# Kernel optimization log

Measured on AMD Instinct MI355X. Metric: run time of the kernel, lower is better.

Reference implementation:

```python
import jax, jax.numpy as jnp
import numpy as np

N_NODES = 100000
N_EDGES = 1600000
IN_CH = 128
HID = 32
HEADS = 4
OUT_CH = 32
NEG_SLOPE = 0.2  # PyG GATConv default


def setup_inputs() -> dict:
    key = jax.random.key(0)
    ks = jax.random.split(key, 12)
    s = 0.1
    x = jax.random.normal(ks[0], (N_NODES, IN_CH), dtype=jnp.float32)
    edge_index = jax.random.randint(ks[1], (2, N_EDGES), 0, N_NODES, dtype=jnp.int64)
    # layer 1: in -> heads*hid, concat
    W1 = jax.random.normal(ks[2], (IN_CH, HEADS * HID), dtype=jnp.float32) * s
    a_src1 = jax.random.normal(ks[3], (HEADS, HID), dtype=jnp.float32) * s
    a_dst1 = jax.random.normal(ks[4], (HEADS, HID), dtype=jnp.float32) * s
    b1 = jnp.zeros((HEADS * HID,), dtype=jnp.float32)
    # layer 2: heads*hid -> out, single head, averaged
    W2 = jax.random.normal(ks[5], (HEADS * HID, OUT_CH), dtype=jnp.float32) * s
    a_src2 = jax.random.normal(ks[6], (1, OUT_CH), dtype=jnp.float32) * s
    a_dst2 = jax.random.normal(ks[7], (1, OUT_CH), dtype=jnp.float32) * s
    b2 = jnp.zeros((OUT_CH,), dtype=jnp.float32)
    return {"x": x, "edge_index": edge_index, "W1": W1, "a_src1": a_src1,
            "a_dst1": a_dst1, "b1": b1, "W2": W2, "a_src2": a_src2,
            "a_dst2": a_dst2, "b2": b2}


def _gat_layer(x, src, dst, W, a_s, a_d, b, heads, ch, concat):
    n = x.shape[0]
    h = (x @ W).reshape(n, heads, ch)            # [N,H,C]
    alpha_s = jnp.einsum('nhc,hc->nh', h, a_s)   # [N,H]
    alpha_d = jnp.einsum('nhc,hc->nh', h, a_d)
    e = jax.nn.leaky_relu(alpha_s[src] + alpha_d[dst], NEG_SLOPE)  # [E,H]
    # segment softmax over edges sharing a destination (self-loops guarantee
    # every segment is non-empty)
    m = jax.ops.segment_max(e, dst, num_segments=n)
    ex = jnp.exp(e - m[dst])
    denom = jax.ops.segment_sum(ex, dst, num_segments=n)
    alpha = ex / (denom[dst] + 1e-16)            # [E,H]
    out = jax.ops.segment_sum(alpha[:, :, None] * h[src], dst, num_segments=n)  # [N,H,C]
    out = out.reshape(n, heads * ch) if concat else out.mean(axis=1)
    return out + b


def reference(x, edge_index, W1, a_src1, a_dst1, b1, W2, a_src2, a_dst2, b2):
    n = x.shape[0]
    loop = jnp.arange(n, dtype=edge_index.dtype)
    src = jnp.concatenate([edge_index[0], loop])  # add self-loops (PyG default)
    dst = jnp.concatenate([edge_index[1], loop])
    h = _gat_layer(x, src, dst, W1, a_src1, a_dst1, b1, HEADS, HID, True)
    h = jax.nn.relu(h)
    # dropout(p=0.5) is identity in eval mode
    out = _gat_layer(h, src, dst, W2, a_src2, a_dst2, b2, 1, OUT_CH, False)
    return out
```

## Files before the change

kernel.cpp:

```cpp
#include <hip/hip_runtime.h>
#include <math.h>

#define NEG_SLOPE 0.2f
#define EPB 8192

typedef __attribute__((ext_vector_type(8))) short bf16x8;
typedef __attribute__((ext_vector_type(4))) float f32x4;

__device__ __forceinline__ unsigned pack_bf16x2(float a, float b) {
    unsigned ua = __float_as_uint(a);
    unsigned ub = __float_as_uint(b);
    ua += 0x7FFFu + ((ua >> 16) & 1u);
    ub += 0x7FFFu + ((ub >> 16) & 1u);
    return (ua >> 16) | (ub & 0xFFFF0000u);
}
__device__ __forceinline__ unsigned short bf16r(float f) {
    unsigned u = __float_as_uint(f);
    u += 0x7FFFu + ((u >> 16) & 1u);
    return (unsigned short)(u >> 16);
}
__device__ __forceinline__ float bf_lo(unsigned u) { return __uint_as_float(u << 16); }
__device__ __forceinline__ float bf_hi(unsigned u) { return __uint_as_float(u & 0xFFFF0000u); }

#if defined(__has_builtin)
#if __has_builtin(__builtin_amdgcn_make_buffer_rsrc) && \
    __has_builtin(__builtin_amdgcn_raw_ptr_buffer_load_b32) && \
    __has_builtin(__builtin_amdgcn_raw_ptr_buffer_load_b64)
#define USE_BUFLD 1
#endif
#endif

#ifdef USE_BUFLD
typedef __amdgpu_buffer_rsrc_t Rsrc;
typedef __attribute__((ext_vector_type(2))) unsigned uint2v;
__device__ __forceinline__ Rsrc mkrsrc(const void* p) {
    return __builtin_amdgcn_make_buffer_rsrc((void*)p, (short)0, -1, 0x00020000);
}
__device__ __forceinline__ unsigned bufld_u32(Rsrc r, int voff) {
    return __builtin_amdgcn_raw_ptr_buffer_load_b32(r, voff, 0, 0);
}
__device__ __forceinline__ float bufld_f32(Rsrc r, int voff) {
    return __uint_as_float(__builtin_amdgcn_raw_ptr_buffer_load_b32(r, voff, 0, 0));
}
__device__ __forceinline__ uint2 bufld_u64(Rsrc r, int voff) {
    uint2v v = __builtin_amdgcn_raw_ptr_buffer_load_b64(r, voff, 0, 0);
    return make_uint2(v.x, v.y);
}
#else
struct Rsrc { const char* p; };
__device__ __forceinline__ Rsrc mkrsrc(const void* p) { Rsrc r; r.p = (const char*)p; return r; }
__device__ __forceinline__ unsigned bufld_u32(Rsrc r, int voff) { return *(const unsigned*)(r.p + voff); }
__device__ __forceinline__ float bufld_f32(Rsrc r, int voff) { return *(const float*)(r.p + voff); }
__device__ __forceinline__ uint2 bufld_u64(Rsrc r, int voff) { return *(const uint2*)(r.p + voff); }
#endif

#define SWZ(row, byteoff) ((((row) * 256) + (byteoff)) ^ (((row) & 15) << 4))


__global__ __launch_bounds__(256) void wcvt_kernel(const float* __restrict__ W,
                                                   unsigned short* __restrict__ WT,
                                                   int Nc, int total) {
    int id = blockIdx.x * 256 + threadIdx.x;
    if (id < total) {
        int n = id >> 7, k = id & 127;
        WT[id] = bf16r(W[k * Nc + n]);
    }
}


__global__ __launch_bounds__(256) void gscan_bsum(const int* __restrict__ arr,
                                                  int* __restrict__ psum, int M) {
    __shared__ int red[4];
    int tid = threadIdx.x;
    int idx = blockIdx.x * 256 + tid;
    int v = (idx < M) ? arr[idx] : 0;
    #pragma unroll
    for (int off = 1; off < 64; off <<= 1) v += __shfl_xor(v, off, 64);
    if ((tid & 63) == 0) red[tid >> 6] = v;
    __syncthreads();
    if (tid == 0) psum[blockIdx.x] = red[0] + red[1] + red[2] + red[3];
}

__global__ __launch_bounds__(1024) void gscan_psum(int* __restrict__ psum, int nb) {
    __shared__ int ws[16];
    int tid = threadIdx.x, lane = tid & 63, w = tid >> 6;
    int v = (tid < nb) ? psum[tid] : 0;
    int incl = v;
    #pragma unroll
    for (int off = 1; off < 64; off <<= 1) {
        int t = __shfl_up(incl, off, 64);
        if (lane >= off) incl += t;
    }
    if (lane == 63) ws[w] = incl;
    __syncthreads();
    int wbase = 0;
    #pragma unroll
    for (int j = 0; j < 16; j++) { if (j < w) wbase += ws[j]; }
    if (tid < nb) psum[tid] = wbase + incl - v;
}

__global__ __launch_bounds__(256) void gscan_final(int* __restrict__ arr,
                                                   const int* __restrict__ psum, int M) {
    __shared__ int ws[4];
    int tid = threadIdx.x, lane = tid & 63, w = tid >> 6;
    int idx = blockIdx.x * 256 + tid;
    int v = (idx < M) ? arr[idx] : 0;
    int incl = v;
    #pragma unroll
    for (int off = 1; off < 64; off <<= 1) {
        int t = __shfl_up(incl, off, 64);
        if (lane >= off) incl += t;
    }
    if (lane == 63) ws[w] = incl;
    __syncthreads();
    int wbase = 0;
    #pragma unroll
    for (int j = 0; j < 4; j++) { if (j < w) wbase += ws[j]; }
    if (idx < M) arr[idx] = psum[blockIdx.x] + wbase + incl - v;
}


__global__ __launch_bounds__(256) void p1_hist(const int* __restrict__ dst, int E, int N,
                                               int nblk1, int nbuckets,
                                               int* __restrict__ partial) {
    __shared__ int hist[1024];
    int tid = threadIdx.x;
    for (int i = tid; i < nbuckets; i += 256) hist[i] = 0;
    __syncthreads();
    int base = blockIdx.x * EPB;
    int tot = E + N;
    #pragma unroll
    for (int it = 0; it < EPB / 256; it++) {
        int i = base + it * 256 + tid;
        if (i < tot) {
            int d = (i < E) ? dst[i] : (i - E);
            atomicAdd(&hist[d >> 8], 1);
        }
    }
    __syncthreads();
    for (int b = tid; b < nbuckets; b += 256)
        partial[b * nblk1 + blockIdx.x] = hist[b];
}

__global__ __launch_bounds__(256) void p1_scatter(const int* __restrict__ src,
                                                  const int* __restrict__ dst, int E, int N,
                                                  int nblk1, int nbuckets,
                                                  const int* __restrict__ scanned,
                                                  unsigned* __restrict__ pairs) {
    __shared__ int cursor[1024];
    int tid = threadIdx.x;
    for (int b = tid; b < nbuckets; b += 256)
        cursor[b] = scanned[b * nblk1 + blockIdx.x];
    __syncthreads();
    int base = blockIdx.x * EPB;
    int tot = E + N;
    #pragma unroll
    for (int it = 0; it < EPB / 256; it++) {
        int i = base + it * 256 + tid;
        if (i < tot) {
            int s = (i < E) ? src[i] : (i - E);
            int d = (i < E) ? dst[i] : (i - E);
            int pos = atomicAdd(&cursor[d >> 8], 1);
            pairs[pos] = ((unsigned)(d & 255) << 24) | (unsigned)s;
        }
    }
}

#define P2CAP 8192

__global__ __launch_bounds__(256) void p2_kernel(const unsigned* __restrict__ pairs,
                                                 const int* __restrict__ scanned,
                                                 int nblk1, int nbuckets, int Etot, int N,
                                                 int* __restrict__ rowptr,
                                                 int* __restrict__ col) {
    __shared__ unsigned buf[P2CAP];
    __shared__ int cnt[256];
    __shared__ int cur[256];
    __shared__ int wsum[4];
    int b = blockIdx.x;
    int tid = threadIdx.x, lane = tid & 63, w = tid >> 6;
    int bucketStart = scanned[b * nblk1];
    int bucketEnd = (b + 1 < nbuckets) ? scanned[(b + 1) * nblk1] : Etot;
    int sz = bucketEnd - bucketStart;
    bool inLds = (sz <= P2CAP);
    cnt[tid] = 0;
    if (inLds) {
        for (int i = tid; i < sz; i += 256) buf[i] = pairs[bucketStart + i];
    }
    __syncthreads();
    if (inLds) {
        for (int i = tid; i < sz; i += 256) atomicAdd(&cnt[buf[i] >> 24], 1);
    } else {
        for (int i = bucketStart + tid; i < bucketEnd; i += 256)
            atomicAdd(&cnt[pairs[i] >> 24], 1);
    }
    __syncthreads();
    int v = cnt[tid];
    int incl = v;
    #pragma unroll
    for (int off = 1; off < 64; off <<= 1) {
        int t = __shfl_up(incl, off, 64);
        if (lane >= off) incl += t;
    }
    if (lane == 63) wsum[w] = incl;
    __syncthreads();
    int wbase = 0;
    #pragma unroll
    for (int j = 0; j < 4; j++) { if (j < w) wbase += wsum[j]; }
    int base = bucketStart + wbase + incl - v;
    cur[tid] = base;
    int d = b * 256 + tid;
    if (d < N) rowptr[d] = base;
    if (b == nbuckets - 1 && tid == 0) rowptr[N] = Etot;
    __syncthreads();
    if (inLds) {
        for (int i = tid; i < sz; i += 256) {
            unsigned p = buf[i];
            int pos = atomicAdd(&cur[p >> 24], 1);
            col[pos] = (int)(p & 0xFFFFFFu);
        }
    } else {
        for (int i = bucketStart + tid; i < bucketEnd; i += 256) {
            unsigned p = pairs[i];
            int pos = atomicAdd(&cur[p >> 24], 1);
            col[pos] = (int)(p & 0xFFFFFFu);
        }
    }
}


__global__ __launch_bounds__(256) void exk_kernel(const int* __restrict__ rowptr,
                                                  const int* __restrict__ col,
                                                  const float* __restrict__ as1,
                                                  const float4* __restrict__ ad4,
                                                  float* __restrict__ exh,
                                                  int N, int Etot) {
    int lane = threadIdx.x & 63;
    int wid = __builtin_amdgcn_readfirstlane(threadIdx.x >> 6);
    int n = blockIdx.x * 4 + wid;
    if (n >= N) return;
    int h = lane >> 4, jj = lane & 15;
    float4 D = ad4[n];
    float dn = (h < 2) ? (h == 0 ? D.x : D.y) : (h == 2 ? D.z : D.w);
    int beg = rowptr[n], end = rowptr[n + 1];
    int planeBase = h * Etot;
    for (int i = beg; i < end; i += 16) {
        int e = i + jj;
        if (e < end) {
            int s = col[e];
            float a = as1[s * 4 + h];
            float v = a + dn;
            v = fmaxf(v, v * NEG_SLOPE);
            exh[planeBase + e] = __expf(v);
        }
    }
}


__global__ __launch_bounds__(256) void gemm1_kernel(const float* __restrict__ x,
                                                    const unsigned short* __restrict__ W1T,
                                                    const float* __restrict__ a_s,
                                                    const float* __restrict__ a_d,
                                                    uint4* __restrict__ h1b,
                                                    float* __restrict__ as1,
                                                    float* __restrict__ ad1, int N) {
    __shared__ char xs[16384];
    __shared__ char wsm[32768];
    int tid = threadIdx.x;
    int row0 = blockIdx.x * 64;

    #pragma unroll
    for (int it = 0; it < 8; it++) {
        int idx = it * 256 + tid;
        int n = idx >> 4, kq = idx & 15;
        uint4 v = ((const uint4*)W1T)[idx];
        *(uint4*)(wsm + SWZ(n, kq * 16)) = v;
    }
    #pragma unroll
    for (int it = 0; it < 8; it++) {
        int idx = it * 256 + tid;
        int r = idx >> 5, k4 = idx & 31;
        int row = row0 + r;
        float4 v = (row < N) ? ((const float4*)x)[(size_t)row * 32 + k4]
                             : make_float4(0.f, 0.f, 0.f, 0.f);
        uint2 p;
        p.x = pack_bf16x2(v.x, v.y);
        p.y = pack_bf16x2(v.z, v.w);
        *(uint2*)(xs + SWZ(r, k4 * 8)) = p;
    }
    __syncthreads();

    int wv = tid >> 6, lane = tid & 63;
    int r0 = wv * 16;
    int lm = lane & 15, lk = lane >> 4;

    bf16x8 afr[4];
    #pragma unroll
    for (int ks = 0; ks < 4; ks++) {
        int row = r0 + lm;
        afr[ks] = *(const bf16x8*)(xs + SWZ(row, ks * 64 + lk * 16));
    }
    f32x4 acc[8];
    #pragma unroll
    for (int nt = 0; nt < 8; nt++) acc[nt] = (f32x4){0.f, 0.f, 0.f, 0.f};

    #pragma unroll
    for (int nt = 0; nt < 8; nt++) {
        int c = nt * 16 + lm;
        #pragma unroll
        for (int ks = 0; ks < 4; ks++) {
            bf16x8 bfr = *(const bf16x8*)(wsm + SWZ(c, ks * 64 + lk * 16));
            acc[nt] = __builtin_amdgcn_mfma_f32_16x16x32_bf16(afr[ks], bfr, acc[nt], 0, 0, 0);
        }
    }
    __syncthreads();

    #pragma unroll
    for (int nt = 0; nt < 8; nt++) {
        int c = nt * 16 + lm;
        #pragma unroll
        for (int e = 0; e < 4; e++) {
            int row = r0 + lk * 4 + e;
            *(unsigned short*)(xs + SWZ(row, c * 2)) = bf16r(acc[nt][e]);
        }
    }
    __syncthreads();

    #pragma unroll
    for (int it = 0; it < 4; it++) {
        int idx = it * 256 + tid;
        int row = idx >> 4, q = idx & 15;
        if (row0 + row < N) {
            uint4 v = *(const uint4*)(xs + SWZ(row, q * 16));
            h1b[(size_t)(row0 + row) * 16 + q] = v;
        }
    }
    {
        int row = tid >> 2, h = tid & 3;
        if (row0 + row < N) {
            float sd = 0.f, dd = 0.f;
            #pragma unroll
            for (int q = 0; q < 4; q++) {
                uint4 v = *(const uint4*)(xs + SWZ(row, h * 64 + q * 16));
                unsigned uu[4] = {v.x, v.y, v.z, v.w};
                #pragma unroll
                for (int j = 0; j < 4; j++) {
                    int k = h * 32 + q * 8 + 2 * j;
                    sd = fmaf(bf_lo(uu[j]), a_s[k], sd);
                    sd = fmaf(bf_hi(uu[j]), a_s[k + 1], sd);
                    dd = fmaf(bf_lo(uu[j]), a_d[k], dd);
                    dd = fmaf(bf_hi(uu[j]), a_d[k + 1], dd);
                }
            }
            as1[(row0 + row) * 4 + h] = sd;
            ad1[(row0 + row) * 4 + h] = dd;
        }
    }
}


__global__ __launch_bounds__(256) void agg1_kernel(const int* __restrict__ rowptr,
                                                   const int* __restrict__ col,
                                                   const unsigned* __restrict__ h1b,
                                                   const float* __restrict__ exh,
                                                   const float* __restrict__ b1,
                                                   unsigned* __restrict__ out1b,
                                                   int N, int Etot) {
    int lane = threadIdx.x & 63;
    int wid = __builtin_amdgcn_readfirstlane(threadIdx.x >> 6);
    int n = blockIdx.x * 4 + wid;
    if (n >= N) return;
    int hh = lane >> 4;
    Rsrc h1r = mkrsrc(h1b);
    Rsrc exr = mkrsrc(exh);
    int laneByte = lane << 2;
    int exBase = hh * Etot;
    int beg = rowptr[n], end = rowptr[n + 1];
    float ax0 = 0.f, ay0 = 0.f, d0 = 0.f;
    float ax1 = 0.f, ay1 = 0.f, d1 = 0.f;
    float ax2 = 0.f, ay2 = 0.f, d2 = 0.f;
    float ax3 = 0.f, ay3 = 0.f, d3 = 0.f;
    int i = beg;
    for (; i + 16 <= end; i += 16) {
        unsigned uu[16];
        float ex[16];
        #pragma unroll
        for (int j = 0; j < 16; j++) {
            int s = col[i + j];
            uu[j] = bufld_u32(h1r, (s << 8) + laneByte);
            ex[j] = bufld_f32(exr, (exBase + i + j) << 2);
        }
        #pragma unroll
        for (int j = 0; j < 16; j += 4) {
            d0 += ex[j];     ax0 = fmaf(ex[j],     bf_lo(uu[j]),     ax0); ay0 = fmaf(ex[j],     bf_hi(uu[j]),     ay0);
            d1 += ex[j + 1]; ax1 = fmaf(ex[j + 1], bf_lo(uu[j + 1]), ax1); ay1 = fmaf(ex[j + 1], bf_hi(uu[j + 1]), ay1);
            d2 += ex[j + 2]; ax2 = fmaf(ex[j + 2], bf_lo(uu[j + 2]), ax2); ay2 = fmaf(ex[j + 2], bf_hi(uu[j + 2]), ay2);
            d3 += ex[j + 3]; ax3 = fmaf(ex[j + 3], bf_lo(uu[j + 3]), ax3); ay3 = fmaf(ex[j + 3], bf_hi(uu[j + 3]), ay3);
        }
    }
    for (; i + 4 <= end; i += 4) {
        unsigned uu[4];
        float ex[4];
        #pragma unroll
        for (int j = 0; j < 4; j++) {
            int s = col[i + j];
            uu[j] = bufld_u32(h1r, (s << 8) + laneByte);
            ex[j] = bufld_f32(exr, (exBase + i + j) << 2);
        }
        d0 += ex[0]; ax0 = fmaf(ex[0], bf_lo(uu[0]), ax0); ay0 = fmaf(ex[0], bf_hi(uu[0]), ay0);
        d1 += ex[1]; ax1 = fmaf(ex[1], bf_lo(uu[1]), ax1); ay1 = fmaf(ex[1], bf_hi(uu[1]), ay1);
        d2 += ex[2]; ax2 = fmaf(ex[2], bf_lo(uu[2]), ax2); ay2 = fmaf(ex[2], bf_hi(uu[2]), ay2);
        d3 += ex[3]; ax3 = fmaf(ex[3], bf_lo(uu[3]), ax3); ay3 = fmaf(ex[3], bf_hi(uu[3]), ay3);
    }
    for (; i < end; i++) {
        int s = col[i];
        unsigned u = bufld_u32(h1r, (s << 8) + laneByte);
        float x = bufld_f32(exr, (exBase + i) << 2);
        d0 += x;
        ax0 = fmaf(x, bf_lo(u), ax0);
        ay0 = fmaf(x, bf_hi(u), ay0);
    }
    float den = (d0 + d1) + (d2 + d3);
    float ax = (ax0 + ax1) + (ax2 + ax3);
    float ay = (ay0 + ay1) + (ay2 + ay3);
    float2 bb = ((const float2*)b1)[lane];
    float ox = fmaxf(ax / den + bb.x, 0.f);
    float oy = fmaxf(ay / den + bb.y, 0.f);
    out1b[n * 64 + lane] = pack_bf16x2(ox, oy);
}


__global__ __launch_bounds__(256) void gemm2_kernel(const uint4* __restrict__ out1b,
                                                    const unsigned short* __restrict__ W2T,
                                                    const float* __restrict__ a_s,
                                                    const float* __restrict__ a_d,
                                                    uint4* __restrict__ h2b,
                                                    float* __restrict__ as2,
                                                    float* __restrict__ ad2, int N) {
    __shared__ char xs[16384];
    __shared__ char wsm[8192];
    int tid = threadIdx.x;
    int row0 = blockIdx.x * 64;

    #pragma unroll
    for (int it = 0; it < 2; it++) {
        int idx = it * 256 + tid;
        int n = idx >> 4, kq = idx & 15;
        uint4 v = ((const uint4*)W2T)[idx];
        *(uint4*)(wsm + SWZ(n, kq * 16)) = v;
    }
    #pragma unroll
    for (int it = 0; it < 4; it++) {
        int idx = it * 256 + tid;
        int r = idx >> 4, q = idx & 15;
        int row = row0 + r;
        uint4 v = (row < N) ? out1b[(size_t)row * 16 + q] : make_uint4(0, 0, 0, 0);
        *(uint4*)(xs + SWZ(r, q * 16)) = v;
    }
    __syncthreads();

    int wv = tid >> 6, lane = tid & 63;
    int r0 = wv * 16;
    int lm = lane & 15, lk = lane >> 4;

    bf16x8 afr[4];
    #pragma unroll
    for (int ks = 0; ks < 4; ks++) {
        int row = r0 + lm;
        afr[ks] = *(const bf16x8*)(xs + SWZ(row, ks * 64 + lk * 16));
    }
    f32x4 acc[2];
    acc[0] = (f32x4){0.f, 0.f, 0.f, 0.f};
    acc[1] = (f32x4){0.f, 0.f, 0.f, 0.f};
    #pragma unroll
    for (int nt = 0; nt < 2; nt++) {
        int c = nt * 16 + lm;
        #pragma unroll
        for (int ks = 0; ks < 4; ks++) {
            bf16x8 bfr = *(const bf16x8*)(wsm + SWZ(c, ks * 64 + lk * 16));
            acc[nt] = __builtin_amdgcn_mfma_f32_16x16x32_bf16(afr[ks], bfr, acc[nt], 0, 0, 0);
        }
    }
    __syncthreads();

    #pragma unroll
    for (int nt = 0; nt < 2; nt++) {
        int c = nt * 16 + lm;
        #pragma unroll
        for (int e = 0; e < 4; e++) {
            int row = r0 + lk * 4 + e;
            *(unsigned short*)(xs + SWZ(row, c * 2)) = bf16r(acc[nt][e]);
        }
    }
    __syncthreads();

    {
        int row = tid >> 2, q = tid & 3;
        if (row0 + row < N) {
            uint4 v = *(const uint4*)(xs + SWZ(row, q * 16));
            h2b[(size_t)(row0 + row) * 4 + q] = v;
        }
    }
    if (tid < 64 && row0 + tid < N) {
        float sd = 0.f, dd = 0.f;
        #pragma unroll
        for (int q = 0; q < 4; q++) {
            uint4 v = *(const uint4*)(xs + SWZ(tid, q * 16));
            unsigned uu[4] = {v.x, v.y, v.z, v.w};
            #pragma unroll
            for (int j = 0; j < 4; j++) {
                int k = q * 8 + 2 * j;
                sd = fmaf(bf_lo(uu[j]), a_s[k], sd);
                sd = fmaf(bf_hi(uu[j]), a_s[k + 1], sd);
                dd = fmaf(bf_lo(uu[j]), a_d[k], dd);
                dd = fmaf(bf_hi(uu[j]), a_d[k + 1], dd);
            }
        }
        as2[row0 + tid] = sd;
        ad2[row0 + tid] = dd;
    }
}


#define A2SLOT(u, l)                                               \
    {                                                              \
        float e = l + adn;                                         \
        e = fmaxf(e, e * NEG_SLOPE);                               \
        float ex = __expf(e);                                      \
        den += ex;                                                 \
        a0 = fmaf(ex, bf_lo(u.x), a0);                             \
        a1 = fmaf(ex, bf_hi(u.x), a1);                             \
        a2 = fmaf(ex, bf_lo(u.y), a2);                             \
        a3 = fmaf(ex, bf_hi(u.y), a3);                             \
    }

__global__ __launch_bounds__(256) void agg2_kernel(const int* __restrict__ rowptr,
                                                   const int* __restrict__ col,
                                                   const unsigned* __restrict__ h2b,
                                                   const float* __restrict__ as2,
                                                   const float* __restrict__ ad2,
                                                   const float* __restrict__ b2,
                                                   float* __restrict__ out, int N) {
    int lane = threadIdx.x & 63;
    int wid = __builtin_amdgcn_readfirstlane(threadIdx.x >> 6);
    int n = blockIdx.x * 4 + wid;
    if (n >= N) return;
    int q8 = lane >> 3;
    int cl = lane & 7;
    Rsrc h2r = mkrsrc(h2b);
    Rsrc asr = mkrsrc(as2);
    int clByte = cl << 3;
    float adn = ad2[n];
    int beg = rowptr[n], end = rowptr[n + 1];
    float a0 = 0.f, a1 = 0.f, a2 = 0.f, a3 = 0.f, den = 0.f;
    int i = beg;
    for (; i + 16 <= end; i += 16) {
        int e0 = i + q8, e1 = i + 8 + q8;
        int s0 = col[e0], s1 = col[e1];
        uint2 u0 = bufld_u64(h2r, (s0 << 6) + clByte);
        uint2 u1 = bufld_u64(h2r, (s1 << 6) + clByte);
        float l0 = bufld_f32(asr, s0 << 2);
        float l1 = bufld_f32(asr, s1 << 2);
        A2SLOT(u0, l0) A2SLOT(u1, l1)
    }
    for (; i < end; i += 8) {
        int e = i + q8;
        if (e < end) {
            int s = col[e];
            uint2 u = bufld_u64(h2r, (s << 6) + clByte);
            float l = bufld_f32(asr, s << 2);
            A2SLOT(u, l)
        }
    }
    den += __shfl_xor(den, 8, 64);
    den += __shfl_xor(den, 16, 64);
    den += __shfl_xor(den, 32, 64);
    a0 += __shfl_xor(a0, 8, 64);  a0 += __shfl_xor(a0, 16, 64);  a0 += __shfl_xor(a0, 32, 64);
    a1 += __shfl_xor(a1, 8, 64);  a1 += __shfl_xor(a1, 16, 64);  a1 += __shfl_xor(a1, 32, 64);
    a2 += __shfl_xor(a2, 8, 64);  a2 += __shfl_xor(a2, 16, 64);  a2 += __shfl_xor(a2, 32, 64);
    a3 += __shfl_xor(a3, 8, 64);  a3 += __shfl_xor(a3, 16, 64);  a3 += __shfl_xor(a3, 32, 64);
    if (q8 == 0) {
        float4 bb = ((const float4*)b2)[cl];
        float4 o;
        o.x = a0 / den + bb.x;
        o.y = a1 / den + bb.y;
        o.z = a2 / den + bb.z;
        o.w = a3 / den + bb.w;
        ((float4*)out)[n * 8 + cl] = o;
    }
}


extern "C" void kernel_launch(void* const* d_in, const int* in_sizes, int n_in,
                              void* d_out, int out_size, void* d_ws, size_t ws_size,
                              hipStream_t stream) {
    const float* x    = (const float*)d_in[0];
    const int*   ei   = (const int*)d_in[1];
    const float* W1   = (const float*)d_in[2];
    const float* a_s1 = (const float*)d_in[3];
    const float* a_d1 = (const float*)d_in[4];
    const float* b1   = (const float*)d_in[5];
    const float* W2   = (const float*)d_in[6];
    const float* a_s2 = (const float*)d_in[7];
    const float* a_d2 = (const float*)d_in[8];
    const float* b2   = (const float*)d_in[9];

    int N = in_sizes[0] / 128;
    int E = in_sizes[1] / 2;
    const int* srcA = ei;
    const int* dstA = ei + E;
    int Etot = E + N;

    char* ws = (char*)d_ws;
    size_t off = 0;
    auto alloc = [&](size_t bytes) {
        void* p = ws + off;
        off += (bytes + 255) & ~(size_t)255;
        return p;
    };
    unsigned* h1b   = (unsigned*)alloc((size_t)N * 128 * 2);
    unsigned* out1b = (unsigned*)alloc((size_t)N * 128 * 2);
    unsigned* h2b   = (unsigned*)alloc((size_t)N * 32 * 2);
    float* as1      = (float*)alloc((size_t)N * 4 * 4);
    float* ad1      = (float*)alloc((size_t)N * 4 * 4);
    float* as2      = (float*)alloc((size_t)N * 4);
    float* ad2      = (float*)alloc((size_t)N * 4);
    int*   rowptr   = (int*)alloc((size_t)(N + 1) * 4);
    int*   col      = (int*)alloc((size_t)Etot * 4);
    unsigned* pairs = (unsigned*)alloc((size_t)Etot * 4);
    float* exh      = (float*)alloc((size_t)Etot * 4 * 4);
    unsigned short* W1T = (unsigned short*)alloc(128 * 128 * 2);
    unsigned short* W2T = (unsigned short*)alloc(32 * 128 * 2);

    int nbuckets = (N + 255) >> 8;
    int nblk1 = (Etot + EPB - 1) / EPB;
    int M = nbuckets * nblk1;
    int*   partial = (int*)alloc((size_t)M * 4);
    int nbs = (M + 255) / 256;
    int*   psum    = (int*)alloc((size_t)1024 * 4);

    hipLaunchKernelGGL(wcvt_kernel, dim3(64), dim3(256), 0, stream, W1, W1T, 128, 16384);
    hipLaunchKernelGGL(wcvt_kernel, dim3(16), dim3(256), 0, stream, W2, W2T, 32, 4096);
    hipLaunchKernelGGL(gemm1_kernel, dim3((N + 63) / 64), dim3(256), 0, stream,
                       x, W1T, a_s1, a_d1, (uint4*)h1b, as1, ad1, N);

    hipLaunchKernelGGL(p1_hist, dim3(nblk1), dim3(256), 0, stream,
                       dstA, E, N, nblk1, nbuckets, partial);
    hipLaunchKernelGGL(gscan_bsum, dim3(nbs), dim3(256), 0, stream, partial, psum, M);
    hipLaunchKernelGGL(gscan_psum, dim3(1), dim3(1024), 0, stream, psum, nbs);
    hipLaunchKernelGGL(gscan_final, dim3(nbs), dim3(256), 0, stream, partial, psum, M);
    hipLaunchKernelGGL(p1_scatter, dim3(nblk1), dim3(256), 0, stream,
                       srcA, dstA, E, N, nblk1, nbuckets, partial, pairs);
    hipLaunchKernelGGL(p2_kernel, dim3(nbuckets), dim3(256), 0, stream,
                       pairs, partial, nblk1, nbuckets, Etot, N, rowptr, col);

    hipLaunchKernelGGL(exk_kernel, dim3((N + 3) / 4), dim3(256), 0, stream,
                       rowptr, col, as1, (const float4*)ad1, exh, N, Etot);

    hipLaunchKernelGGL(agg1_kernel, dim3((N + 3) / 4), dim3(256), 0, stream,
                       rowptr, col, h1b, exh, b1, out1b, N, Etot);
    hipLaunchKernelGGL(gemm2_kernel, dim3((N + 63) / 64), dim3(256), 0, stream,
                       (const uint4*)out1b, W2T, a_s2, a_d2, (uint4*)h2b, as2, ad2, N);
    hipLaunchKernelGGL(agg2_kernel, dim3((N + 3) / 4), dim3(256), 0, stream,
                       rowptr, col, h2b, as2, ad2, b2, (float*)d_out, N);
}
```

Measured before the change: 235.0 us.

## Fuse edge exp computation into layer-1 aggregation and merge weight conversion kernels

Removes the separate exk_kernel, which wrote per-edge, per-head exp scores to a 4*E float buffer, and instead recomputes leaky-relu and exp inside agg1 from as1[src] and ad1[dst]. This drops a kernel launch plus a roughly 27 MB write and reread, at the cost of an extra gathered 4-byte load and an exp per edge-lane in agg1. It also merges the two weight-conversion launches into one and makes row bounds wave-uniform with readfirstlane in both aggregation kernels.

```diff
diff --git a/kernel.cpp b/kernel.cpp
--- a/kernel.cpp
+++ b/kernel.cpp
@@ -57,13 +57,18 @@
 #define SWZ(row, byteoff) ((((row) * 256) + (byteoff)) ^ (((row) & 15) << 4))
 
 
-__global__ __launch_bounds__(256) void wcvt_kernel(const float* __restrict__ W,
-                                                   unsigned short* __restrict__ WT,
-                                                   int Nc, int total) {
+__global__ __launch_bounds__(256) void wcvt_kernel(const float* __restrict__ W1,
+                                                   const float* __restrict__ W2,
+                                                   unsigned short* __restrict__ W1T,
+                                                   unsigned short* __restrict__ W2T) {
     int id = blockIdx.x * 256 + threadIdx.x;
-    if (id < total) {
+    if (id < 16384) {
         int n = id >> 7, k = id & 127;
-        WT[id] = bf16r(W[k * Nc + n]);
+        W1T[id] = bf16r(W1[k * 128 + n]);
+    } else if (id < 20480) {
+        int j = id - 16384;
+        int n = j >> 7, k = j & 127;
+        W2T[j] = bf16r(W2[k * 32 + n]);
     }
 }
 
@@ -224,34 +229,6 @@
             unsigned p = pairs[i];
             int pos = atomicAdd(&cur[p >> 24], 1);
             col[pos] = (int)(p & 0xFFFFFFu);
-        }
-    }
-}
-
-
-__global__ __launch_bounds__(256) void exk_kernel(const int* __restrict__ rowptr,
-                                                  const int* __restrict__ col,
-                                                  const float* __restrict__ as1,
-                                                  const float4* __restrict__ ad4,
-                                                  float* __restrict__ exh,
-                                                  int N, int Etot) {
-    int lane = threadIdx.x & 63;
-    int wid = __builtin_amdgcn_readfirstlane(threadIdx.x >> 6);
-    int n = blockIdx.x * 4 + wid;
-    if (n >= N) return;
-    int h = lane >> 4, jj = lane & 15;
-    float4 D = ad4[n];
-    float dn = (h < 2) ? (h == 0 ? D.x : D.y) : (h == 2 ? D.z : D.w);
-    int beg = rowptr[n], end = rowptr[n + 1];
-    int planeBase = h * Etot;
-    for (int i = beg; i < end; i += 16) {
-        int e = i + jj;
-        if (e < end) {
-            int s = col[e];
-            float a = as1[s * 4 + h];
-            float v = a + dn;
-            v = fmaxf(v, v * NEG_SLOPE);
-            exh[planeBase + e] = __expf(v);
         }
     }
 }
@@ -362,63 +339,81 @@
 __global__ __launch_bounds__(256) void agg1_kernel(const int* __restrict__ rowptr,
                                                    const int* __restrict__ col,
                                                    const unsigned* __restrict__ h1b,
-                                                   const float* __restrict__ exh,
+                                                   const float* __restrict__ as1,
+                                                   const float* __restrict__ ad1,
                                                    const float* __restrict__ b1,
-                                                   unsigned* __restrict__ out1b,
-                                                   int N, int Etot) {
+                                                   unsigned* __restrict__ out1b, int N) {
     int lane = threadIdx.x & 63;
     int wid = __builtin_amdgcn_readfirstlane(threadIdx.x >> 6);
     int n = blockIdx.x * 4 + wid;
     if (n >= N) return;
     int hh = lane >> 4;
+    float adn = ad1[n * 4 + hh];
     Rsrc h1r = mkrsrc(h1b);
-    Rsrc exr = mkrsrc(exh);
+    Rsrc asr = mkrsrc(as1);
     int laneByte = lane << 2;
-    int exBase = hh * Etot;
-    int beg = rowptr[n], end = rowptr[n + 1];
+    int hhByte = hh << 2;
+    int beg = __builtin_amdgcn_readfirstlane(rowptr[n]);
+    int end = __builtin_amdgcn_readfirstlane(rowptr[n + 1]);
     float ax0 = 0.f, ay0 = 0.f, d0 = 0.f;
     float ax1 = 0.f, ay1 = 0.f, d1 = 0.f;
     float ax2 = 0.f, ay2 = 0.f, d2 = 0.f;
     float ax3 = 0.f, ay3 = 0.f, d3 = 0.f;
     int i = beg;
     for (; i + 16 <= end; i += 16) {
+        int ss[16];
         unsigned uu[16];
-        float ex[16];
+        float ll[16];
+        #pragma unroll
+        for (int j = 0; j < 16; j++) ss[j] = col[i + j];
         #pragma unroll
         for (int j = 0; j < 16; j++) {
-            int s = col[i + j];
-            uu[j] = bufld_u32(h1r, (s << 8) + laneByte);
-            ex[j] = bufld_f32(exr, (exBase + i + j) << 2);
-        }
-        #pragma unroll
-        for (int j = 0; j < 16; j += 4) {
-            d0 += ex[j];     ax0 = fmaf(ex[j],     bf_lo(uu[j]),     ax0); ay0 = fmaf(ex[j],     bf_hi(uu[j]),     ay0);
-            d1 += ex[j + 1]; ax1 = fmaf(ex[j + 1], bf_lo(uu[j + 1]), ax1); ay1 = fmaf(ex[j + 1], bf_hi(uu[j + 1]), ay1);
-            d2 += ex[j + 2]; ax2 = fmaf(ex[j + 2], bf_lo(uu[j + 2]), ax2); ay2 = fmaf(ex[j + 2], bf_hi(uu[j + 2]), ay2);
-            d3 += ex[j + 3]; ax3 = fmaf(ex[j + 3], bf_lo(uu[j + 3]), ax3); ay3 = fmaf(ex[j + 3], bf_hi(uu[j + 3]), ay3);
+            uu[j] = bufld_u32(h1r, (ss[j] << 8) + laneByte);
+            ll[j] = bufld_f32(asr, (ss[j] << 4) + hhByte);
+        }
+        #pragma unroll
+        for (int j = 0; j < 16; j++) {
+            float e = ll[j] + adn;
+            e = fmaxf(e, e * NEG_SLOPE);
+            float ex = __expf(e);
+            if ((j & 3) == 0)      { d0 += ex; ax0 = fmaf(ex, bf_lo(uu[j]), ax0); ay0 = fmaf(ex, bf_hi(uu[j]), ay0); }
+            else if ((j & 3) == 1) { d1 += ex; ax1 = fmaf(ex, bf_lo(uu[j]), ax1); ay1 = fmaf(ex, bf_hi(uu[j]), ay1); }
+            else if ((j & 3) == 2) { d2 += ex; ax2 = fmaf(ex, bf_lo(uu[j]), ax2); ay2 = fmaf(ex, bf_hi(uu[j]), ay2); }
+            else                   { d3 += ex; ax3 = fmaf(ex, bf_lo(uu[j]), ax3); ay3 = fmaf(ex, bf_hi(uu[j]), ay3); }
         }
     }
     for (; i + 4 <= end; i += 4) {
+        int ss[4];
         unsigned uu[4];
-        float ex[4];
+        float ll[4];
+        #pragma unroll
+        for (int j = 0; j < 4; j++) ss[j] = col[i + j];
         #pragma unroll
         for (int j = 0; j < 4; j++) {
-            int s = col[i + j];
-            uu[j] = bufld_u32(h1r, (s << 8) + laneByte);
-            ex[j] = bufld_f32(exr, (exBase + i + j) << 2);
-        }
-        d0 += ex[0]; ax0 = fmaf(ex[0], bf_lo(uu[0]), ax0); ay0 = fmaf(ex[0], bf_hi(uu[0]), ay0);
-        d1 += ex[1]; ax1 = fmaf(ex[1], bf_lo(uu[1]), ax1); ay1 = fmaf(ex[1], bf_hi(uu[1]), ay1);
-        d2 += ex[2]; ax2 = fmaf(ex[2], bf_lo(uu[2]), ax2); ay2 = fmaf(ex[2], bf_hi(uu[2]), ay2);
-        d3 += ex[3]; ax3 = fmaf(ex[3], bf_lo(uu[3]), ax3); ay3 = fmaf(ex[3], bf_hi(uu[3]), ay3);
+            uu[j] = bufld_u32(h1r, (ss[j] << 8) + laneByte);
+            ll[j] = bufld_f32(asr, (ss[j] << 4) + hhByte);
+        }
+        #pragma unroll
+        for (int j = 0; j < 4; j++) {
+            float e = ll[j] + adn;
+            e = fmaxf(e, e * NEG_SLOPE);
+            float ex = __expf(e);
+            if (j == 0)      { d0 += ex; ax0 = fmaf(ex, bf_lo(uu[j]), ax0); ay0 = fmaf(ex, bf_hi(uu[j]), ay0); }
+            else if (j == 1) { d1 += ex; ax1 = fmaf(ex, bf_lo(uu[j]), ax1); ay1 = fmaf(ex, bf_hi(uu[j]), ay1); }
+            else if (j == 2) { d2 += ex; ax2 = fmaf(ex, bf_lo(uu[j]), ax2); ay2 = fmaf(ex, bf_hi(uu[j]), ay2); }
+            else             { d3 += ex; ax3 = fmaf(ex, bf_lo(uu[j]), ax3); ay3 = fmaf(ex, bf_hi(uu[j]), ay3); }
+        }
     }
     for (; i < end; i++) {
         int s = col[i];
         unsigned u = bufld_u32(h1r, (s << 8) + laneByte);
-        float x = bufld_f32(exr, (exBase + i) << 2);
-        d0 += x;
-        ax0 = fmaf(x, bf_lo(u), ax0);
-        ay0 = fmaf(x, bf_hi(u), ay0);
+        float l = bufld_f32(asr, (s << 4) + hhByte);
+        float e = l + adn;
+        e = fmaxf(e, e * NEG_SLOPE);
+        float ex = __expf(e);
+        d0 += ex;
+        ax0 = fmaf(ex, bf_lo(u), ax0);
+        ay0 = fmaf(ex, bf_hi(u), ay0);
     }
     float den = (d0 + d1) + (d2 + d3);
     float ax = (ax0 + ax1) + (ax2 + ax3);
@@ -551,7 +546,8 @@
     Rsrc asr = mkrsrc(as2);
     int clByte = cl << 3;
     float adn = ad2[n];
-    int beg = rowptr[n], end = rowptr[n + 1];
+    int beg = __builtin_amdgcn_readfirstlane(rowptr[n]);
+    int end = __builtin_amdgcn_readfirstlane(rowptr[n + 1]);
     float a0 = 0.f, a1 = 0.f, a2 = 0.f, a3 = 0.f, den = 0.f;
     int i = beg;
     for (; i + 16 <= end; i += 16) {
@@ -628,7 +624,6 @@
     int*   rowptr   = (int*)alloc((size_t)(N + 1) * 4);
     int*   col      = (int*)alloc((size_t)Etot * 4);
     unsigned* pairs = (unsigned*)alloc((size_t)Etot * 4);
-    float* exh      = (float*)alloc((size_t)Etot * 4 * 4);
     unsigned short* W1T = (unsigned short*)alloc(128 * 128 * 2);
     unsigned short* W2T = (unsigned short*)alloc(32 * 128 * 2);
 
@@ -639,8 +634,7 @@
     int nbs = (M + 255) / 256;
     int*   psum    = (int*)alloc((size_t)1024 * 4);
 
-    hipLaunchKernelGGL(wcvt_kernel, dim3(64), dim3(256), 0, stream, W1, W1T, 128, 16384);
-    hipLaunchKernelGGL(wcvt_kernel, dim3(16), dim3(256), 0, stream, W2, W2T, 32, 4096);
+    hipLaunchKernelGGL(wcvt_kernel, dim3(80), dim3(256), 0, stream, W1, W2, W1T, W2T);
     hipLaunchKernelGGL(gemm1_kernel, dim3((N + 63) / 64), dim3(256), 0, stream,
                        x, W1T, a_s1, a_d1, (uint4*)h1b, as1, ad1, N);
 
@@ -654,11 +648,8 @@
     hipLaunchKernelGGL(p2_kernel, dim3(nbuckets), dim3(256), 0, stream,
                        pairs, partial, nblk1, nbuckets, Etot, N, rowptr, col);
 
-    hipLaunchKernelGGL(exk_kernel, dim3((N + 3) / 4), dim3(256), 0, stream,
-                       rowptr, col, as1, (const float4*)ad1, exh, N, Etot);
-
     hipLaunchKernelGGL(agg1_kernel, dim3((N + 3) / 4), dim3(256), 0, stream,
-                       rowptr, col, h1b, exh, b1, out1b, N, Etot);
+                       rowptr, col, h1b, as1, ad1, b1, out1b, N);
     hipLaunchKernelGGL(gemm2_kernel, dim3((N + 63) / 64), dim3(256), 0, stream,
                        (const uint4*)out1b, W2T, a_s2, a_d2, (uint4*)h2b, as2, ad2, N);
     hipLaunchKernelGGL(agg2_kernel, dim3((N + 3) / 4), dim3(256), 0, stream,
```

Measured after the change: 211.6 us. 1.11x faster.
